# Kernel optimization log

Hardware: AMD Instinct MI355X
Metric: run time of the kernel (lower is better)

Reference implementation:

```python
import jax, jax.numpy as jnp
import numpy as np

N, E, D, K, PDIM = 100000, 1600000, 64, 4, 2
EPS = 1e-15


def setup_inputs() -> dict:
    key = jax.random.key(0)
    k1, k2, k3, k4, k5, k6 = jax.random.split(key, 6)
    x = jax.random.normal(k1, (N, D), dtype=jnp.float32)
    edge_index = jax.random.randint(k2, (2, E), 0, N, dtype=jnp.int64)
    g = jax.random.normal(k3, (D, K * D), dtype=jnp.float32) / np.sqrt(D)
    mu = jax.random.normal(k4, (K, PDIM), dtype=jnp.float32)
    sigma = jax.random.uniform(k5, (K, PDIM), dtype=jnp.float32, minval=0.5, maxval=1.5)
    root = jax.random.normal(k6, (D, D), dtype=jnp.float32) / np.sqrt(D)
    bias = jnp.zeros((D,), dtype=jnp.float32)
    return {"x": x, "edge_index": edge_index, "g": g, "mu": mu,
            "sigma": sigma, "root": root, "bias": bias}


def reference(x, edge_index, g, mu, sigma, root, bias):
    src, dst = edge_index[0], edge_index[1]
    n = x.shape[0]
    # in-degree; used for pseudo-coords and mean aggregation
    deg = jax.ops.segment_sum(jnp.ones((src.shape[0],), x.dtype), dst, num_segments=n)
    deg = jnp.maximum(deg, 1.0)
    inv_sqrt_deg = jax.lax.rsqrt(deg)
    # pseudo-coordinates per edge: [E, 2]
    pseudo = jnp.stack([inv_sqrt_deg[src], inv_sqrt_deg[dst]], axis=-1)
    # Gaussian mixture weights: [E, K]
    diff = pseudo[:, None, :] - mu[None, :, :]              # [E, K, 2]
    gw = jnp.exp(jnp.sum(-0.5 * diff * diff / (EPS + sigma * sigma)[None], axis=-1))
    # per-kernel transformed features: [N, K, D]
    xt = (x @ g).reshape(n, K, -1)
    agg = jnp.zeros((n, xt.shape[-1]), x.dtype)
    for k in range(K):  # small fixed K=4; keeps per-edge intermediate at [E, D]
        msg = gw[:, k, None] * xt[src, k]
        agg = agg + jax.ops.segment_sum(msg, dst, num_segments=n)
    agg = agg / deg[:, None]                                # mean aggregation
    conv = agg + x @ root + bias
    return x + jax.nn.relu(conv)
```

## Files before the change

### kernel.cpp

```cpp
#include <hip/hip_runtime.h>

#define EPS 1e-15f
#define CAP 32
#define HSTR 272

typedef __attribute__((ext_vector_type(8))) short short8;
typedef __attribute__((ext_vector_type(4))) float f32x4;

__device__ __forceinline__ unsigned short f2bf(float f) {
    unsigned u = __float_as_uint(f);
    u = (u + 0x7FFF + ((u >> 16) & 1)) >> 16;
    return (unsigned short)u;
}
__device__ __forceinline__ float bf2f(unsigned short h) {
    return __uint_as_float(((unsigned)h) << 16);
}

__global__ void k_fill2(const int* __restrict__ ei, int E, int* __restrict__ cnt,
                        int* __restrict__ csrp, int* __restrict__ ovf,
                        int* __restrict__ ovfcnt) {
    int e = blockIdx.x * blockDim.x + threadIdx.x;
    if (e < E) {
        int src = ei[e];
        int dst = ei[E + e];
        int slot = atomicAdd(&cnt[dst], 1);
        if (slot < CAP) {
            csrp[dst * CAP + slot] = src;
        } else {
            int o = atomicAdd(ovfcnt, 1);
            ovf[2 * o] = src;
            ovf[2 * o + 1] = dst;
        }
    }
}

__global__ void k_AB(const int* __restrict__ cnt, const float* __restrict__ mu,
                     const float* __restrict__ sigma,
                     float4* __restrict__ A4, float4* __restrict__ B4, int n) {
    int i = blockIdx.x * 256 + threadIdx.x;
    if (i >= n) return;
    int c = cnt[i];
    float v = rsqrtf((float)(c > 1 ? c : 1));
    float a[4], b[4];
    #pragma unroll
    for (int k = 0; k < 4; ++k) {
        float s0 = sigma[2 * k], s1 = sigma[2 * k + 1];
        float w0 = -0.5f / (EPS + s0 * s0);
        float w1 = -0.5f / (EPS + s1 * s1);
        float d0 = v - mu[2 * k];
        float d1 = v - mu[2 * k + 1];
        a[k] = __expf(d0 * d0 * w0);
        b[k] = __expf(d1 * d1 * w1);
    }
    A4[i] = (float4){a[0], a[1], a[2], a[3]};
    B4[i] = (float4){b[0], b[1], b[2], b[3]};
}

__global__ void k_packB(const float* __restrict__ g, const float* __restrict__ root,
                        unsigned short* __restrict__ Bhi, unsigned short* __restrict__ Blo) {
    int idx = blockIdx.x * 256 + threadIdx.x;
    if (idx >= 20480) return;
    int i  = idx & 7;
    int l  = (idx >> 3) & 63;
    int ct = idx >> 9;
    int c = ct >> 2, t = ct & 3;
    int kk = c * 32 + ((l >> 4) & 3) * 8 + i;
    int j  = t * 16 + (l & 15);
    float v = (kk < 256) ? g[(kk & 63) * 256 + (kk >> 6) * 64 + j]
                         : root[(kk - 256) * 64 + j];
    unsigned short hi = f2bf(v);
    unsigned short lo = f2bf(v - bf2f(hi));
    Bhi[idx] = hi;
    Blo[idx] = lo;
}

__global__ __launch_bounds__(256, 8) void k_fused(
    const int* __restrict__ cnt, const int* __restrict__ csrp,
    const int* __restrict__ ovf, const int* __restrict__ ovfcnt,
    const float4* __restrict__ A4, const float4* __restrict__ B4,
    const float* __restrict__ x,
    const unsigned short* __restrict__ Bhi, const unsigned short* __restrict__ Blo,
    const float* __restrict__ bias, float* __restrict__ out, int n) {
    __shared__ float hs[16 * HSTR];
    const int lane = threadIdx.x & 63;
    const int w    = threadIdx.x >> 6;
    const int r0   = blockIdx.x * 16;

    for (int q = 0; q < 4; ++q) {
        const int nd   = w * 4 + q;
        const int node = r0 + nd;
        float a0 = 0.f, a1 = 0.f, a2 = 0.f, a3 = 0.f;
        if (node < n) {
            const int len = cnt[node];
            const int m   = len < CAP ? len : CAP;
            const int* cp = csrp + (size_t)node * CAP;
            if (m > 0) {
                int    s_cur  = cp[0];
                float4 A_cur  = A4[s_cur];
                float  xv_cur = x[(size_t)s_cur * 64 + lane];
                int    s_nxt  = (m > 1) ? cp[1] : s_cur;
                for (int j = 0; j < m; ++j) {
                    int    s_n2 = (j + 2 < m) ? cp[j + 2] : s_nxt;
                    float4 A_n  = A4[s_nxt];
                    float  xv_n = x[(size_t)s_nxt * 64 + lane];
                    a0 = fmaf(A_cur.x, xv_cur, a0);
                    a1 = fmaf(A_cur.y, xv_cur, a1);
                    a2 = fmaf(A_cur.z, xv_cur, a2);
                    a3 = fmaf(A_cur.w, xv_cur, a3);
                    A_cur = A_n; xv_cur = xv_n; s_nxt = s_n2;
                }
            }
            if (len > CAP) {
                const int no = *ovfcnt;
                for (int j = 0; j < no; ++j) {
                    int od = ovf[2 * j + 1];
                    if (od == node) {
                        int os = ovf[2 * j];
                        float4 Av = A4[os];
                        float  xv = x[(size_t)os * 64 + lane];
                        a0 = fmaf(Av.x, xv, a0);
                        a1 = fmaf(Av.y, xv, a1);
                        a2 = fmaf(Av.z, xv, a2);
                        a3 = fmaf(Av.w, xv, a3);
                    }
                }
            }
            const float invd = 1.0f / (float)(len > 1 ? len : 1);
            float4 Bv = B4[node];
            hs[nd * HSTR + lane]       = a0 * (Bv.x * invd);
            hs[nd * HSTR + 64 + lane]  = a1 * (Bv.y * invd);
            hs[nd * HSTR + 128 + lane] = a2 * (Bv.z * invd);
            hs[nd * HSTR + 192 + lane] = a3 * (Bv.w * invd);
        } else {
            hs[nd * HSTR + lane]       = 0.f;
            hs[nd * HSTR + 64 + lane]  = 0.f;
            hs[nd * HSTR + 128 + lane] = 0.f;
            hs[nd * HSTR + 192 + lane] = 0.f;
        }
    }
    __syncthreads();

    const int t     = w;
    const int arow  = r0 + (lane & 15);
    const int arowc = arow < n ? arow : n - 1;
    const int kgrp  = (lane >> 4) * 8;
    f32x4 acc = (f32x4){0.f, 0.f, 0.f, 0.f};

    #pragma unroll
    for (int c = 0; c < 10; ++c) {
        float av[8];
        if (c < 8) {
            const float* ap = &hs[(lane & 15) * HSTR + c * 32 + kgrp];
            float4 p0 = *reinterpret_cast<const float4*>(ap);
            float4 p1 = *reinterpret_cast<const float4*>(ap + 4);
            av[0]=p0.x; av[1]=p0.y; av[2]=p0.z; av[3]=p0.w;
            av[4]=p1.x; av[5]=p1.y; av[6]=p1.z; av[7]=p1.w;
        } else {
            const float* ap = x + (size_t)arowc * 64 + (c - 8) * 32 + kgrp;
            float4 p0 = *reinterpret_cast<const float4*>(ap);
            float4 p1 = *reinterpret_cast<const float4*>(ap + 4);
            av[0]=p0.x; av[1]=p0.y; av[2]=p0.z; av[3]=p0.w;
            av[4]=p1.x; av[5]=p1.y; av[6]=p1.z; av[7]=p1.w;
        }
        short8 ahi, alo;
        #pragma unroll
        for (int i = 0; i < 8; ++i) {
            unsigned short hi = f2bf(av[i]);
            ahi[i] = (short)hi;
            alo[i] = (short)f2bf(av[i] - bf2f(hi));
        }
        const int boff = ((c * 4 + t) * 64 + lane) * 8;
        short8 bhi = *reinterpret_cast<const short8*>(Bhi + boff);
        short8 blo = *reinterpret_cast<const short8*>(Blo + boff);
        acc = __builtin_amdgcn_mfma_f32_16x16x32_bf16(ahi, bhi, acc, 0, 0, 0);
        acc = __builtin_amdgcn_mfma_f32_16x16x32_bf16(alo, bhi, acc, 0, 0, 0);
        acc = __builtin_amdgcn_mfma_f32_16x16x32_bf16(ahi, blo, acc, 0, 0, 0);
    }

    const int lq  = (lane >> 4) * 4;
    const int col = t * 16 + (lane & 15);
    const float bv = bias[col];
    #pragma unroll
    for (int q = 0; q < 4; ++q) {
        const int row = r0 + lq + q;
        if (row < n) {
            const size_t o = (size_t)row * 64 + col;
            float xres = x[o];
            float conv = acc[q] + bv;
            out[o] = xres + (conv > 0.f ? conv : 0.f);
        }
    }
}

extern "C" void kernel_launch(void* const* d_in, const int* in_sizes, int n_in,
                              void* d_out, int out_size, void* d_ws, size_t ws_size,
                              hipStream_t stream) {
    const float* x     = (const float*)d_in[0];
    const int*   ei    = (const int*)d_in[1];
    const float* g     = (const float*)d_in[2];
    const float* mu    = (const float*)d_in[3];
    const float* sigma = (const float*)d_in[4];
    const float* root  = (const float*)d_in[5];
    const float* bias  = (const float*)d_in[6];
    float* out = (float*)d_out;

    const int n = in_sizes[0] / 64;
    const int E = in_sizes[1] / 2;

    int* cnt    = (int*)d_ws;
    int* ovfcnt = cnt + n;
    unsigned short* Bhi = (unsigned short*)(ovfcnt + 4);
    unsigned short* Blo = Bhi + 20480;
    float4* A4  = (float4*)(Blo + 20480);
    float4* B4  = A4 + n;
    int* csrp   = (int*)(B4 + n);
    int* ovf    = csrp + (size_t)n * CAP;

    hipMemsetAsync(cnt, 0, (size_t)n * sizeof(int), stream);
    hipMemsetAsync(ovfcnt, 0, 4 * sizeof(int), stream);

    k_fill2<<<(E + 255) / 256, 256, 0, stream>>>(ei, E, cnt, csrp, ovf, ovfcnt);
    k_AB<<<(n + 255) / 256, 256, 0, stream>>>(cnt, mu, sigma, A4, B4, n);
    k_packB<<<80, 256, 0, stream>>>(g, root, Bhi, Blo);
    const int nstrip = (n + 15) / 16;
    k_fused<<<nstrip, 256, 0, stream>>>(cnt, csrp, ovf, ovfcnt, A4, B4, x,
                                        Bhi, Blo, bias, out, n);
}
```

Baseline: 380.2 us.

## Partition CSR fill by destination range and stage bf16 hi/lo splits in LDS

```diff
diff --git a/kernel.cpp b/kernel.cpp
--- a/kernel.cpp
+++ b/kernel.cpp
@@ -2,7 +2,8 @@
 
 #define EPS 1e-15f
 #define CAP 32
-#define HSTR 272
+#define NP 4
+#define HS2 264
 
 typedef __attribute__((ext_vector_type(8))) short short8;
 typedef __attribute__((ext_vector_type(4))) float f32x4;
@@ -16,20 +17,22 @@
     return __uint_as_float(((unsigned)h) << 16);
 }
 
-__global__ void k_fill2(const int* __restrict__ ei, int E, int* __restrict__ cnt,
-                        int* __restrict__ csrp, int* __restrict__ ovf,
-                        int* __restrict__ ovfcnt) {
+__global__ void k_fill2(const int* __restrict__ ei, int E, int dlo, int dhi,
+                        int* __restrict__ cnt, int* __restrict__ csrp,
+                        int* __restrict__ ovf, int* __restrict__ ovfcnt) {
     int e = blockIdx.x * blockDim.x + threadIdx.x;
     if (e < E) {
-        int src = ei[e];
         int dst = ei[E + e];
-        int slot = atomicAdd(&cnt[dst], 1);
-        if (slot < CAP) {
-            csrp[dst * CAP + slot] = src;
-        } else {
-            int o = atomicAdd(ovfcnt, 1);
-            ovf[2 * o] = src;
-            ovf[2 * o + 1] = dst;
+        if (dst >= dlo && dst < dhi) {
+            int src = ei[e];
+            int slot = atomicAdd(&cnt[dst], 1);
+            if (slot < CAP) {
+                csrp[dst * CAP + slot] = src;
+            } else {
+                int o = atomicAdd(ovfcnt, 1);
+                ovf[2 * o] = src;
+                ovf[2 * o + 1] = dst;
+            }
         }
     }
 }
@@ -81,7 +84,8 @@
     const float* __restrict__ x,
     const unsigned short* __restrict__ Bhi, const unsigned short* __restrict__ Blo,
     const float* __restrict__ bias, float* __restrict__ out, int n) {
-    __shared__ float hs[16 * HSTR];
+    __shared__ unsigned short hsH[16 * HS2];
+    __shared__ unsigned short hsL[16 * HS2];
     const int lane = threadIdx.x & 63;
     const int w    = threadIdx.x >> 6;
     const int r0   = blockIdx.x * 16;
@@ -90,6 +94,7 @@
         const int nd   = w * 4 + q;
         const int node = r0 + nd;
         float a0 = 0.f, a1 = 0.f, a2 = 0.f, a3 = 0.f;
+        float sc0 = 0.f, sc1 = 0.f, sc2 = 0.f, sc3 = 0.f;
         if (node < n) {
             const int len = cnt[node];
             const int m   = len < CAP ? len : CAP;
@@ -127,16 +132,16 @@
             }
             const float invd = 1.0f / (float)(len > 1 ? len : 1);
             float4 Bv = B4[node];
-            hs[nd * HSTR + lane]       = a0 * (Bv.x * invd);
-            hs[nd * HSTR + 64 + lane]  = a1 * (Bv.y * invd);
-            hs[nd * HSTR + 128 + lane] = a2 * (Bv.z * invd);
-            hs[nd * HSTR + 192 + lane] = a3 * (Bv.w * invd);
-        } else {
-            hs[nd * HSTR + lane]       = 0.f;
-            hs[nd * HSTR + 64 + lane]  = 0.f;
-            hs[nd * HSTR + 128 + lane] = 0.f;
-            hs[nd * HSTR + 192 + lane] = 0.f;
-        }
+            sc0 = Bv.x * invd; sc1 = Bv.y * invd;
+            sc2 = Bv.z * invd; sc3 = Bv.w * invd;
+        }
+        float v0 = a0 * sc0, v1 = a1 * sc1, v2 = a2 * sc2, v3 = a3 * sc3;
+        const int hb = nd * HS2;
+        unsigned short u0 = f2bf(v0), u1 = f2bf(v1), u2 = f2bf(v2), u3 = f2bf(v3);
+        hsH[hb + lane]       = u0;  hsL[hb + lane]       = f2bf(v0 - bf2f(u0));
+        hsH[hb + 64 + lane]  = u1;  hsL[hb + 64 + lane]  = f2bf(v1 - bf2f(u1));
+        hsH[hb + 128 + lane] = u2;  hsL[hb + 128 + lane] = f2bf(v2 - bf2f(u2));
+        hsH[hb + 192 + lane] = u3;  hsL[hb + 192 + lane] = f2bf(v3 - bf2f(u3));
     }
     __syncthreads();
 
@@ -148,26 +153,22 @@
 
     #pragma unroll
     for (int c = 0; c < 10; ++c) {
-        float av[8];
+        short8 ahi, alo;
         if (c < 8) {
-            const float* ap = &hs[(lane & 15) * HSTR + c * 32 + kgrp];
-            float4 p0 = *reinterpret_cast<const float4*>(ap);
-            float4 p1 = *reinterpret_cast<const float4*>(ap + 4);
-            av[0]=p0.x; av[1]=p0.y; av[2]=p0.z; av[3]=p0.w;
-            av[4]=p1.x; av[5]=p1.y; av[6]=p1.z; av[7]=p1.w;
+            const int off = (lane & 15) * HS2 + c * 32 + kgrp;
+            ahi = *reinterpret_cast<const short8*>(&hsH[off]);
+            alo = *reinterpret_cast<const short8*>(&hsL[off]);
         } else {
             const float* ap = x + (size_t)arowc * 64 + (c - 8) * 32 + kgrp;
             float4 p0 = *reinterpret_cast<const float4*>(ap);
             float4 p1 = *reinterpret_cast<const float4*>(ap + 4);
-            av[0]=p0.x; av[1]=p0.y; av[2]=p0.z; av[3]=p0.w;
-            av[4]=p1.x; av[5]=p1.y; av[6]=p1.z; av[7]=p1.w;
-        }
-        short8 ahi, alo;
-        #pragma unroll
-        for (int i = 0; i < 8; ++i) {
-            unsigned short hi = f2bf(av[i]);
-            ahi[i] = (short)hi;
-            alo[i] = (short)f2bf(av[i] - bf2f(hi));
+            float av[8] = {p0.x, p0.y, p0.z, p0.w, p1.x, p1.y, p1.z, p1.w};
+            #pragma unroll
+            for (int i = 0; i < 8; ++i) {
+                unsigned short hi = f2bf(av[i]);
+                ahi[i] = (short)hi;
+                alo[i] = (short)f2bf(av[i] - bf2f(hi));
+            }
         }
         const int boff = ((c * 4 + t) * 64 + lane) * 8;
         short8 bhi = *reinterpret_cast<const short8*>(Bhi + boff);
@@ -219,7 +220,12 @@
     hipMemsetAsync(cnt, 0, (size_t)n * sizeof(int), stream);
     hipMemsetAsync(ovfcnt, 0, 4 * sizeof(int), stream);
 
-    k_fill2<<<(E + 255) / 256, 256, 0, stream>>>(ei, E, cnt, csrp, ovf, ovfcnt);
+    const int chunk = (n + NP - 1) / NP;
+    for (int p = 0; p < NP; ++p) {
+        int dlo = p * chunk;
+        int dhi = dlo + chunk < n ? dlo + chunk : n;
+        k_fill2<<<(E + 255) / 256, 256, 0, stream>>>(ei, E, dlo, dhi, cnt, csrp, ovf, ovfcnt);
+    }
     k_AB<<<(n + 255) / 256, 256, 0, stream>>>(cnt, mu, sigma, A4, B4, n);
     k_packB<<<80, 256, 0, stream>>>(g, root, Bhi, Blo);
     const int nstrip = (n + 15) / 16;
```

Result: faster. 357.2 us (-6.0%).
